# Kernel optimization log

Hardware: AMD Instinct MI355X
Metric: run time of the kernel (lower is better)

Reference implementation:

```python
import jax, jax.numpy as jnp
import numpy as np

B, T, N_EMBD, HEAD = 8, 2048, 1024, 64

def setup_inputs() -> dict:
    key = jax.random.key(0)
    kx, kk, kq, kv = jax.random.split(key, 4)
    x = jax.random.normal(kx, (B, T, N_EMBD), dtype=jnp.float32)
    Wk = jax.random.normal(kk, (HEAD, N_EMBD), dtype=jnp.float32) * 0.02
    Wq = jax.random.normal(kq, (HEAD, N_EMBD), dtype=jnp.float32) * 0.02
    Wv = jax.random.normal(kv, (HEAD, N_EMBD), dtype=jnp.float32) * 0.02
    return {"x": x, "Wk": Wk, "Wq": Wq, "Wv": Wv}

def reference(x, Wk, Wq, Wv):
    # x: [B, T, C]; Linear(n_embd, head_size, bias=False) => x @ W.T
    Bq, Tq, C = x.shape
    q = jnp.einsum('btc,hc->bth', x, Wq)  # [B, T, H]
    k = jnp.einsum('btc,hc->bth', x, Wk)
    v = jnp.einsum('btc,hc->bth', x, Wv)
    # NOTE: source scales by C**0.5 with C = n_embd (not head_size); preserved.
    scale = 1.0 / jnp.sqrt(jnp.float32(C))
    wei = jnp.einsum('bth,bsh->bts', q, k) * scale  # [B, T, T]
    # causal mask: allow key position s <= query position t
    causal = jnp.tril(jnp.ones((Tq, Tq), dtype=bool))
    wei = jnp.where(causal[None, :, :], wei, -jnp.inf)
    wei = jax.nn.softmax(wei, axis=-1)
    # dropout is identity at inference
    out = jnp.einsum('bts,bsh->bth', wei, v)  # [B, T, H]
    return out
```

## Files before the change

kernel.cpp:

```cpp
#include <hip/hip_runtime.h>

#define TB 2048
#define NB 8
#define CEMB 1024
#define HD 64
#define BT (NB*TB)
#define QSCALE 0.04508422f

typedef __attribute__((ext_vector_type(8))) short bf16x8;
typedef __attribute__((ext_vector_type(4))) short bf16x4;
typedef __attribute__((ext_vector_type(4))) float f32x4;

#define MFMA32(a, b, c) __builtin_amdgcn_mfma_f32_16x16x32_bf16(a, b, c, 0, 0, 0)
#define MFMA16(a, b, c) __builtin_amdgcn_mfma_f32_16x16x16bf16_1k(a, b, c, 0, 0, 0)

__device__ inline short f2bf(float f) {
    union { float f; unsigned u; } v; v.f = f;
    unsigned r = v.u + 0x7fffu + ((v.u >> 16) & 1u);
    return (short)(r >> 16);
}
__device__ inline float bf2f(short s) {
    union { unsigned u; float f; } v; v.u = ((unsigned)(unsigned short)s) << 16;
    return v.f;
}

__global__ __launch_bounds__(256) void wpack(const float* __restrict__ Wk,
                                             const float* __restrict__ Wq,
                                             const float* __restrict__ Wv,
                                             short* __restrict__ W2) {
    int c = blockIdx.x * 256 + threadIdx.x;
    int lane = c & 63, ntk = c >> 6;
    int nt = ntk % 12, kc = ntk / 12;
    int n = nt * 16 + (lane & 15);
    int col = kc * 32 + (lane >> 4) * 8;
    const float* src = (n < 64) ? Wk + n * 1024
                     : (n < 128) ? Wq + (n - 64) * 1024
                                 : Wv + (n - 128) * 1024;
    float4 a = *(const float4*)(src + col);
    float4 b = *(const float4*)(src + col + 4);
    bf16x8 o;
    o[0] = f2bf(a.x); o[1] = f2bf(a.y); o[2] = f2bf(a.z); o[3] = f2bf(a.w);
    o[4] = f2bf(b.x); o[5] = f2bf(b.y); o[6] = f2bf(b.z); o[7] = f2bf(b.w);
    *(bf16x8*)(W2 + (size_t)c * 8) = o;
}

__global__ __launch_bounds__(256) void qkv_proj(const float* __restrict__ x,
                                                const short* __restrict__ W2,
                                                short* __restrict__ Qb,
                                                short* __restrict__ Kb,
                                                short* __restrict__ Vt) {
    __shared__ short4 Lred[4][3][3][64];
    int tid = threadIdx.x, wave = tid >> 6, lane = tid & 63;
    int l15 = lane & 15, quad = lane >> 4;
    int m0 = blockIdx.x * 16;
    int mrow = m0 + l15;

    f32x4 acc[12];
#pragma unroll
    for (int i = 0; i < 12; ++i) acc[i] = f32x4{0.f, 0.f, 0.f, 0.f};

    const float4* xb4 = (const float4*)(x + (size_t)mrow * CEMB + wave * 256) + quad * 2;
    float4 xq[6];
    xq[0] = xb4[0];  xq[1] = xb4[1];
    xq[2] = xb4[8];  xq[3] = xb4[9];
    xq[4] = xb4[16]; xq[5] = xb4[17];

    const short* wbase = W2 + ((size_t)(wave * 8) * 12 * 64 + lane) * 8;
    bf16x8 wA[12], wB[12];
#pragma unroll
    for (int nt = 0; nt < 12; ++nt)
        wA[nt] = *(const bf16x8*)(wbase + nt * 512);

#pragma unroll
    for (int kc = 0; kc < 8; ++kc) {
        float4 x0 = xq[(kc % 3) * 2], x1 = xq[(kc % 3) * 2 + 1];
        if (kc + 1 < 8) {
            const short* wn = wbase + (size_t)(kc + 1) * 6144;
            if (kc & 1) {
#pragma unroll
                for (int nt = 0; nt < 12; ++nt) wA[nt] = *(const bf16x8*)(wn + nt * 512);
            } else {
#pragma unroll
                for (int nt = 0; nt < 12; ++nt) wB[nt] = *(const bf16x8*)(wn + nt * 512);
            }
        }
        if (kc + 3 < 8) {
            xq[((kc + 3) % 3) * 2]     = xb4[(kc + 3) * 8];
            xq[((kc + 3) % 3) * 2 + 1] = xb4[(kc + 3) * 8 + 1];
        }
        bf16x8 af;
        af[0] = f2bf(x0.x); af[1] = f2bf(x0.y); af[2] = f2bf(x0.z); af[3] = f2bf(x0.w);
        af[4] = f2bf(x1.x); af[5] = f2bf(x1.y); af[6] = f2bf(x1.z); af[7] = f2bf(x1.w);
        if (kc & 1) {
#pragma unroll
            for (int nt = 0; nt < 12; ++nt) acc[nt] = MFMA32(af, wB[nt], acc[nt]);
        } else {
#pragma unroll
            for (int nt = 0; nt < 12; ++nt) acc[nt] = MFMA32(af, wA[nt], acc[nt]);
        }
    }

#pragma unroll
    for (int nt = 0; nt < 12; ++nt) {
        int o = nt / 3;
        if (o != wave) {
            int rank = wave - (wave > o ? 1 : 0);
            short4 p;
            p.x = f2bf(acc[nt][0]); p.y = f2bf(acc[nt][1]);
            p.z = f2bf(acc[nt][2]); p.w = f2bf(acc[nt][3]);
            Lred[o][rank][nt % 3][lane] = p;
        }
    }
    __syncthreads();

    int b = blockIdx.x >> 7;
    int sblk = (m0 & 2047) >> 4;
#pragma unroll
    for (int nt = 0; nt < 12; ++nt) {
        if (wave == nt / 3) {
            f32x4 s = acc[nt];
#pragma unroll
            for (int rk = 0; rk < 3; ++rk) {
                short4 p = Lred[nt / 3][rk][nt % 3][lane];
                s[0] += bf2f(p.x); s[1] += bf2f(p.y);
                s[2] += bf2f(p.z); s[3] += bf2f(p.w);
            }
            if (nt < 4) {
                int h = nt * 16 + l15;
#pragma unroll
                for (int r = 0; r < 4; ++r)
                    Kb[(size_t)(m0 + quad * 4 + r) * HD + h] = f2bf(s[r]);
            } else if (nt < 8) {
                int h = (nt - 4) * 16 + l15;
#pragma unroll
                for (int r = 0; r < 4; ++r)
                    Qb[(size_t)(m0 + quad * 4 + r) * HD + h] = f2bf(s[r] * QSCALE);
            } else {
                int h = (nt - 8) * 16 + l15;
                short4 o4;
                o4.x = f2bf(s[0]); o4.y = f2bf(s[1]); o4.z = f2bf(s[2]); o4.w = f2bf(s[3]);
                *(short4*)(Vt + ((size_t)(b * 128 + sblk) * 64 + h) * 16 + quad * 4) = o4;
            }
        }
    }
}

__global__ __launch_bounds__(256) void flash(const short* __restrict__ Qb,
                                             const short* __restrict__ Kb,
                                             const short* __restrict__ Vt,
                                             float* __restrict__ out) {
    __shared__ float Of[4][16][68];
    __shared__ float Ml[4][16];
    int tid = threadIdx.x, wave = tid >> 6, lane = tid & 63;
    int l15 = lane & 15, quad = lane >> 4;
    int i = blockIdx.x;
    int round = i >> 8, s = i & 255;
    int b = round * 2 + (s & 1);
    int q = (round & 1) ? 127 - (s >> 1) : (s >> 1);
    int tq0 = q * 16;
    size_t bT = (size_t)b * TB;

    const short* qrow = Qb + (bT + tq0 + l15) * HD;
    bf16x8 qf0 = *(const bf16x8*)(qrow + quad * 8);
    bf16x8 qf1 = *(const bf16x8*)(qrow + 32 + quad * 8);

    bf16x4 ones4;
#pragma unroll
    for (int j = 0; j < 4; ++j) ones4[j] = (short)0x3F80;

    f32x4 accO[4];
#pragma unroll
    for (int k = 0; k < 4; ++k) accO[k] = f32x4{0.f, 0.f, 0.f, 0.f};
    f32x4 accL = f32x4{0.f, 0.f, 0.f, 0.f};

    int ntiles = (q + 4) >> 2;
    const short* kbase = Kb + bT * HD;
    const short* vtb = Vt + (size_t)b * 131072;

    int myt = wave;
    if (myt < ntiles) {
        bf16x8 kf[8];
        {
            const short* kr = kbase + (size_t)(myt * 64 + l15) * HD + quad * 8;
#pragma unroll
            for (int st = 0; st < 4; ++st) {
                kf[st * 2]     = *(const bf16x8*)(kr + (size_t)st * 16 * HD);
                kf[st * 2 + 1] = *(const bf16x8*)(kr + (size_t)st * 16 * HD + 32);
            }
        }
        for (; myt < ntiles; myt += 4) {
            int s0 = myt * 64;
            bf16x4 vf[16];
#pragma unroll
            for (int g = 0; g < 4; ++g) {
                int sb = (s0 >> 4) + g;
#pragma unroll
                for (int ht = 0; ht < 4; ++ht)
                    vf[g * 4 + ht] = *(const bf16x4*)(vtb + ((size_t)(sb * 64 + ht * 16 + l15)) * 16 + quad * 4);
            }
            f32x4 sv[4];
#pragma unroll
            for (int st = 0; st < 4; ++st) {
                f32x4 sacc = f32x4{0.f, 0.f, 0.f, 0.f};
                sacc = MFMA32(kf[st * 2], qf0, sacc);
                sacc = MFMA32(kf[st * 2 + 1], qf1, sacc);
                sv[st] = sacc;
            }
            if (myt + 4 < ntiles) {
                const short* kr = kbase + (size_t)(s0 + 256 + l15) * HD + quad * 8;
#pragma unroll
                for (int st = 0; st < 4; ++st) {
                    kf[st * 2]     = *(const bf16x8*)(kr + (size_t)st * 16 * HD);
                    kf[st * 2 + 1] = *(const bf16x8*)(kr + (size_t)st * 16 * HD + 32);
                }
            }
            bool full = (s0 + 64 <= tq0);
            int tg = tq0 + l15;
            bf16x4 pk[4];
#pragma unroll
            for (int st = 0; st < 4; ++st) {
#pragma unroll
                for (int r = 0; r < 4; ++r) {
                    int sg = s0 + st * 16 + quad * 4 + r;
                    float e = (full || sg <= tg) ? __builtin_amdgcn_exp2f(sv[st][r]) : 0.f;
                    pk[st][r] = f2bf(e);
                }
            }
#pragma unroll
            for (int g = 0; g < 4; ++g) {
                accL = MFMA16(ones4, pk[g], accL);
#pragma unroll
                for (int ht = 0; ht < 4; ++ht)
                    accO[ht] = MFMA16(vf[g * 4 + ht], pk[g], accO[ht]);
            }
        }
    }

#pragma unroll
    for (int ht = 0; ht < 4; ++ht) {
        float4 o4;
        o4.x = accO[ht][0]; o4.y = accO[ht][1]; o4.z = accO[ht][2]; o4.w = accO[ht][3];
        *(float4*)&Of[wave][l15][ht * 16 + quad * 4] = o4;
    }
    if (quad == 0) Ml[wave][l15] = accL[0];
    __syncthreads();

    int row = tid >> 4, c4 = (tid & 15) * 4;
    float L = Ml[0][row] + Ml[1][row] + Ml[2][row] + Ml[3][row];
    float inv = 1.0f / L;
    float4 p0 = *(const float4*)&Of[0][row][c4];
    float4 p1 = *(const float4*)&Of[1][row][c4];
    float4 p2 = *(const float4*)&Of[2][row][c4];
    float4 p3 = *(const float4*)&Of[3][row][c4];
    float4 o;
    o.x = (p0.x + p1.x + p2.x + p3.x) * inv;
    o.y = (p0.y + p1.y + p2.y + p3.y) * inv;
    o.z = (p0.z + p1.z + p2.z + p3.z) * inv;
    o.w = (p0.w + p1.w + p2.w + p3.w) * inv;
    *(float4*)(out + (bT + tq0 + row) * HD + c4) = o;
}

extern "C" void kernel_launch(void* const* d_in, const int* in_sizes, int n_in,
                              void* d_out, int out_size, void* d_ws, size_t ws_size,
                              hipStream_t stream) {
    const float* x  = (const float*)d_in[0];
    const float* Wk = (const float*)d_in[1];
    const float* Wq = (const float*)d_in[2];
    const float* Wv = (const float*)d_in[3];
    float* out = (float*)d_out;

    short* W2 = (short*)d_ws;
    short* Qb = W2 + 192 * 1024;
    short* Kb = Qb + (size_t)BT * HD;
    short* Vt = Kb + (size_t)BT * HD;

    wpack<<<96, 256, 0, stream>>>(Wk, Wq, Wv, W2);
    qkv_proj<<<1024, 256, 0, stream>>>(x, W2, Qb, Kb, Vt);
    flash<<<1024, 256, 0, stream>>>(Qb, Kb, Vt, out);
}
```

Before: 156.6 us.

## Process 32 rows per block in projection and attention to reuse weights and K/V

Both the QKV projection and the flash kernel now handle two 16-row tiles per block, so each loaded weight fragment or K/V tile feeds twice as many MFMAs. Grids are halved to 512 blocks. The V-transpose layout moves to 32-key blocks, which allows 16-byte loads. Causal masking is now decided per 16-key subtile, and the projection drops its double-buffered weight prefetch. The trade-offs are higher register pressure, fewer blocks for load balance and occupancy, and more exposed weight-load latency.

```diff
diff --git a/kernel.cpp b/kernel.cpp
--- a/kernel.cpp
+++ b/kernel.cpp
@@ -49,97 +49,96 @@
                                                 short* __restrict__ Qb,
                                                 short* __restrict__ Kb,
                                                 short* __restrict__ Vt) {
-    __shared__ short4 Lred[4][3][3][64];
+    __shared__ short4 Lred[4][3][6][64];
     int tid = threadIdx.x, wave = tid >> 6, lane = tid & 63;
     int l15 = lane & 15, quad = lane >> 4;
-    int m0 = blockIdx.x * 16;
-    int mrow = m0 + l15;
-
-    f32x4 acc[12];
-#pragma unroll
-    for (int i = 0; i < 12; ++i) acc[i] = f32x4{0.f, 0.f, 0.f, 0.f};
-
-    const float4* xb4 = (const float4*)(x + (size_t)mrow * CEMB + wave * 256) + quad * 2;
-    float4 xq[6];
-    xq[0] = xb4[0];  xq[1] = xb4[1];
-    xq[2] = xb4[8];  xq[3] = xb4[9];
-    xq[4] = xb4[16]; xq[5] = xb4[17];
+    int m0 = blockIdx.x * 32;
+
+    f32x4 acc[24];
+#pragma unroll
+    for (int i = 0; i < 24; ++i) acc[i] = f32x4{0.f, 0.f, 0.f, 0.f};
+
+    const float4* xA = (const float4*)(x + (size_t)(m0 + l15) * CEMB + wave * 256) + quad * 2;
+    const float4* xB = (const float4*)(x + (size_t)(m0 + 16 + l15) * CEMB + wave * 256) + quad * 2;
+    float4 xq[8];
+    xq[0] = xA[0]; xq[1] = xA[1]; xq[2] = xB[0]; xq[3] = xB[1];
+    xq[4] = xA[8]; xq[5] = xA[9]; xq[6] = xB[8]; xq[7] = xB[9];
 
     const short* wbase = W2 + ((size_t)(wave * 8) * 12 * 64 + lane) * 8;
-    bf16x8 wA[12], wB[12];
-#pragma unroll
-    for (int nt = 0; nt < 12; ++nt)
-        wA[nt] = *(const bf16x8*)(wbase + nt * 512);
-
 #pragma unroll
     for (int kc = 0; kc < 8; ++kc) {
-        float4 x0 = xq[(kc % 3) * 2], x1 = xq[(kc % 3) * 2 + 1];
-        if (kc + 1 < 8) {
-            const short* wn = wbase + (size_t)(kc + 1) * 6144;
-            if (kc & 1) {
-#pragma unroll
-                for (int nt = 0; nt < 12; ++nt) wA[nt] = *(const bf16x8*)(wn + nt * 512);
-            } else {
-#pragma unroll
-                for (int nt = 0; nt < 12; ++nt) wB[nt] = *(const bf16x8*)(wn + nt * 512);
-            }
-        }
-        if (kc + 3 < 8) {
-            xq[((kc + 3) % 3) * 2]     = xb4[(kc + 3) * 8];
-            xq[((kc + 3) % 3) * 2 + 1] = xb4[(kc + 3) * 8 + 1];
-        }
-        bf16x8 af;
-        af[0] = f2bf(x0.x); af[1] = f2bf(x0.y); af[2] = f2bf(x0.z); af[3] = f2bf(x0.w);
-        af[4] = f2bf(x1.x); af[5] = f2bf(x1.y); af[6] = f2bf(x1.z); af[7] = f2bf(x1.w);
-        if (kc & 1) {
-#pragma unroll
-            for (int nt = 0; nt < 12; ++nt) acc[nt] = MFMA32(af, wB[nt], acc[nt]);
-        } else {
-#pragma unroll
-            for (int nt = 0; nt < 12; ++nt) acc[nt] = MFMA32(af, wA[nt], acc[nt]);
+        bf16x8 wf[12];
+#pragma unroll
+        for (int nt = 0; nt < 12; ++nt)
+            wf[nt] = *(const bf16x8*)(wbase + (size_t)kc * 6144 + nt * 512);
+        int base = (kc & 1) * 4;
+        float4 a0 = xq[base], a1 = xq[base + 1];
+        float4 b0 = xq[base + 2], b1 = xq[base + 3];
+        if (kc + 2 < 8) {
+            xq[base]     = xA[(kc + 2) * 8]; xq[base + 1] = xA[(kc + 2) * 8 + 1];
+            xq[base + 2] = xB[(kc + 2) * 8]; xq[base + 3] = xB[(kc + 2) * 8 + 1];
+        }
+        bf16x8 af0, af1;
+        af0[0] = f2bf(a0.x); af0[1] = f2bf(a0.y); af0[2] = f2bf(a0.z); af0[3] = f2bf(a0.w);
+        af0[4] = f2bf(a1.x); af0[5] = f2bf(a1.y); af0[6] = f2bf(a1.z); af0[7] = f2bf(a1.w);
+        af1[0] = f2bf(b0.x); af1[1] = f2bf(b0.y); af1[2] = f2bf(b0.z); af1[3] = f2bf(b0.w);
+        af1[4] = f2bf(b1.x); af1[5] = f2bf(b1.y); af1[6] = f2bf(b1.z); af1[7] = f2bf(b1.w);
+#pragma unroll
+        for (int nt = 0; nt < 12; ++nt) {
+            acc[nt * 2]     = MFMA32(af0, wf[nt], acc[nt * 2]);
+            acc[nt * 2 + 1] = MFMA32(af1, wf[nt], acc[nt * 2 + 1]);
         }
     }
 
 #pragma unroll
     for (int nt = 0; nt < 12; ++nt) {
-        int o = nt / 3;
-        if (o != wave) {
-            int rank = wave - (wave > o ? 1 : 0);
-            short4 p;
-            p.x = f2bf(acc[nt][0]); p.y = f2bf(acc[nt][1]);
-            p.z = f2bf(acc[nt][2]); p.w = f2bf(acc[nt][3]);
-            Lred[o][rank][nt % 3][lane] = p;
+#pragma unroll
+        for (int mt = 0; mt < 2; ++mt) {
+            int o = nt / 3;
+            if (o != wave) {
+                int rank = wave - (wave > o ? 1 : 0);
+                short4 p;
+                p.x = f2bf(acc[nt * 2 + mt][0]); p.y = f2bf(acc[nt * 2 + mt][1]);
+                p.z = f2bf(acc[nt * 2 + mt][2]); p.w = f2bf(acc[nt * 2 + mt][3]);
+                Lred[o][rank][(nt % 3) * 2 + mt][lane] = p;
+            }
         }
     }
     __syncthreads();
 
-    int b = blockIdx.x >> 7;
-    int sblk = (m0 & 2047) >> 4;
+    int b = blockIdx.x >> 6;
+    int sblk32 = blockIdx.x & 63;
 #pragma unroll
     for (int nt = 0; nt < 12; ++nt) {
         if (wave == nt / 3) {
-            f32x4 s = acc[nt];
+            f32x4 s0 = acc[nt * 2], s1 = acc[nt * 2 + 1];
 #pragma unroll
             for (int rk = 0; rk < 3; ++rk) {
-                short4 p = Lred[nt / 3][rk][nt % 3][lane];
-                s[0] += bf2f(p.x); s[1] += bf2f(p.y);
-                s[2] += bf2f(p.z); s[3] += bf2f(p.w);
+                short4 p0 = Lred[nt / 3][rk][(nt % 3) * 2][lane];
+                short4 p1 = Lred[nt / 3][rk][(nt % 3) * 2 + 1][lane];
+                s0[0] += bf2f(p0.x); s0[1] += bf2f(p0.y); s0[2] += bf2f(p0.z); s0[3] += bf2f(p0.w);
+                s1[0] += bf2f(p1.x); s1[1] += bf2f(p1.y); s1[2] += bf2f(p1.z); s1[3] += bf2f(p1.w);
             }
             if (nt < 4) {
                 int h = nt * 16 + l15;
 #pragma unroll
-                for (int r = 0; r < 4; ++r)
-                    Kb[(size_t)(m0 + quad * 4 + r) * HD + h] = f2bf(s[r]);
+                for (int r = 0; r < 4; ++r) {
+                    Kb[(size_t)(m0 + quad * 4 + r) * HD + h]      = f2bf(s0[r]);
+                    Kb[(size_t)(m0 + 16 + quad * 4 + r) * HD + h] = f2bf(s1[r]);
+                }
             } else if (nt < 8) {
                 int h = (nt - 4) * 16 + l15;
 #pragma unroll
-                for (int r = 0; r < 4; ++r)
-                    Qb[(size_t)(m0 + quad * 4 + r) * HD + h] = f2bf(s[r] * QSCALE);
+                for (int r = 0; r < 4; ++r) {
+                    Qb[(size_t)(m0 + quad * 4 + r) * HD + h]      = f2bf(s0[r] * QSCALE);
+                    Qb[(size_t)(m0 + 16 + quad * 4 + r) * HD + h] = f2bf(s1[r] * QSCALE);
+                }
             } else {
                 int h = (nt - 8) * 16 + l15;
-                short4 o4;
-                o4.x = f2bf(s[0]); o4.y = f2bf(s[1]); o4.z = f2bf(s[2]); o4.w = f2bf(s[3]);
-                *(short4*)(Vt + ((size_t)(b * 128 + sblk) * 64 + h) * 16 + quad * 4) = o4;
+                bf16x8 v8;
+                v8[0] = f2bf(s0[0]); v8[1] = f2bf(s0[1]); v8[2] = f2bf(s0[2]); v8[3] = f2bf(s0[3]);
+                v8[4] = f2bf(s1[0]); v8[5] = f2bf(s1[1]); v8[6] = f2bf(s1[2]); v8[7] = f2bf(s1[3]);
+                *(bf16x8*)(Vt + ((size_t)((b * 64 + sblk32) * 64 + h)) * 32 + quad * 8) = v8;
             }
         }
     }
@@ -149,31 +148,35 @@
                                              const short* __restrict__ Kb,
                                              const short* __restrict__ Vt,
                                              float* __restrict__ out) {
-    __shared__ float Of[4][16][68];
-    __shared__ float Ml[4][16];
+    __shared__ float Of[4][2][16][68];
+    __shared__ float Ml[4][2][16];
     int tid = threadIdx.x, wave = tid >> 6, lane = tid & 63;
     int l15 = lane & 15, quad = lane >> 4;
     int i = blockIdx.x;
     int round = i >> 8, s = i & 255;
-    int b = round * 2 + (s & 1);
-    int q = (round & 1) ? 127 - (s >> 1) : (s >> 1);
-    int tq0 = q * 16;
+    int b = s & 7;
+    int g32 = s >> 3;
+    int q32 = round ? 63 - g32 : g32;
+    int tq0 = q32 * 32;
     size_t bT = (size_t)b * TB;
 
-    const short* qrow = Qb + (bT + tq0 + l15) * HD;
-    bf16x8 qf0 = *(const bf16x8*)(qrow + quad * 8);
-    bf16x8 qf1 = *(const bf16x8*)(qrow + 32 + quad * 8);
+    const short* qr0 = Qb + (bT + tq0 + l15) * HD;
+    const short* qr1 = Qb + (bT + tq0 + 16 + l15) * HD;
+    bf16x8 qf00 = *(const bf16x8*)(qr0 + quad * 8);
+    bf16x8 qf01 = *(const bf16x8*)(qr0 + 32 + quad * 8);
+    bf16x8 qf10 = *(const bf16x8*)(qr1 + quad * 8);
+    bf16x8 qf11 = *(const bf16x8*)(qr1 + 32 + quad * 8);
 
     bf16x4 ones4;
 #pragma unroll
     for (int j = 0; j < 4; ++j) ones4[j] = (short)0x3F80;
 
-    f32x4 accO[4];
-#pragma unroll
-    for (int k = 0; k < 4; ++k) accO[k] = f32x4{0.f, 0.f, 0.f, 0.f};
-    f32x4 accL = f32x4{0.f, 0.f, 0.f, 0.f};
-
-    int ntiles = (q + 4) >> 2;
+    f32x4 accO0[4], accO1[4];
+#pragma unroll
+    for (int k = 0; k < 4; ++k) { accO0[k] = f32x4{0.f,0.f,0.f,0.f}; accO1[k] = f32x4{0.f,0.f,0.f,0.f}; }
+    f32x4 accL0 = f32x4{0.f,0.f,0.f,0.f}, accL1 = f32x4{0.f,0.f,0.f,0.f};
+
+    int ntiles = (tq0 + 95) >> 6;
     const short* kbase = Kb + bT * HD;
     const short* vtb = Vt + (size_t)b * 131072;
 
@@ -190,21 +193,22 @@
         }
         for (; myt < ntiles; myt += 4) {
             int s0 = myt * 64;
-            bf16x4 vf[16];
-#pragma unroll
-            for (int g = 0; g < 4; ++g) {
-                int sb = (s0 >> 4) + g;
+            bf16x8 vf8[8];
+#pragma unroll
+            for (int sb2 = 0; sb2 < 2; ++sb2)
 #pragma unroll
                 for (int ht = 0; ht < 4; ++ht)
-                    vf[g * 4 + ht] = *(const bf16x4*)(vtb + ((size_t)(sb * 64 + ht * 16 + l15)) * 16 + quad * 4);
-            }
-            f32x4 sv[4];
+                    vf8[sb2 * 4 + ht] = *(const bf16x8*)(
+                        vtb + ((size_t)(((s0 >> 5) + sb2) * 64 + ht * 16 + l15)) * 32 + quad * 8);
+            f32x4 sv0[4], sv1[4];
 #pragma unroll
             for (int st = 0; st < 4; ++st) {
-                f32x4 sacc = f32x4{0.f, 0.f, 0.f, 0.f};
-                sacc = MFMA32(kf[st * 2], qf0, sacc);
-                sacc = MFMA32(kf[st * 2 + 1], qf1, sacc);
-                sv[st] = sacc;
+                f32x4 t0 = f32x4{0.f,0.f,0.f,0.f}, t1 = f32x4{0.f,0.f,0.f,0.f};
+                t0 = MFMA32(kf[st * 2], qf00, t0);
+                t0 = MFMA32(kf[st * 2 + 1], qf01, t0);
+                t1 = MFMA32(kf[st * 2], qf10, t1);
+                t1 = MFMA32(kf[st * 2 + 1], qf11, t1);
+                sv0[st] = t0; sv1[st] = t1;
             }
             if (myt + 4 < ntiles) {
                 const short* kr = kbase + (size_t)(s0 + 256 + l15) * HD + quad * 8;
@@ -214,50 +218,65 @@
                     kf[st * 2 + 1] = *(const bf16x8*)(kr + (size_t)st * 16 * HD + 32);
                 }
             }
-            bool full = (s0 + 64 <= tq0);
-            int tg = tq0 + l15;
-            bf16x4 pk[4];
+            int t0g = tq0 + l15, t1g = tq0 + 16 + l15;
+            bf16x4 pk0[4], pk1[4];
 #pragma unroll
             for (int st = 0; st < 4; ++st) {
+                bool full0 = (s0 + st * 16 + 15 <= tq0);
+                bool full1 = (s0 + st * 16 + 15 <= tq0 + 16);
 #pragma unroll
                 for (int r = 0; r < 4; ++r) {
                     int sg = s0 + st * 16 + quad * 4 + r;
-                    float e = (full || sg <= tg) ? __builtin_amdgcn_exp2f(sv[st][r]) : 0.f;
-                    pk[st][r] = f2bf(e);
+                    float e0 = (full0 || sg <= t0g) ? __builtin_amdgcn_exp2f(sv0[st][r]) : 0.f;
+                    float e1 = (full1 || sg <= t1g) ? __builtin_amdgcn_exp2f(sv1[st][r]) : 0.f;
+                    pk0[st][r] = f2bf(e0);
+                    pk1[st][r] = f2bf(e1);
                 }
             }
 #pragma unroll
             for (int g = 0; g < 4; ++g) {
-                accL = MFMA16(ones4, pk[g], accL);
-#pragma unroll
-                for (int ht = 0; ht < 4; ++ht)
-                    accO[ht] = MFMA16(vf[g * 4 + ht], pk[g], accO[ht]);
+                accL0 = MFMA16(ones4, pk0[g], accL0);
+                accL1 = MFMA16(ones4, pk1[g], accL1);
+#pragma unroll
+                for (int ht = 0; ht < 4; ++ht) {
+                    bf16x8 v = vf8[(g >> 1) * 4 + ht];
+                    bf16x4 va;
+                    if (g & 1) { va[0] = v[4]; va[1] = v[5]; va[2] = v[6]; va[3] = v[7]; }
+                    else       { va[0] = v[0]; va[1] = v[1]; va[2] = v[2]; va[3] = v[3]; }
+                    accO0[ht] = MFMA16(va, pk0[g], accO0[ht]);
+                    accO1[ht] = MFMA16(va, pk1[g], accO1[ht]);
+                }
             }
         }
     }
 
 #pragma unroll
     for (int ht = 0; ht < 4; ++ht) {
-        float4 o4;
-        o4.x = accO[ht][0]; o4.y = accO[ht][1]; o4.z = accO[ht][2]; o4.w = accO[ht][3];
-        *(float4*)&Of[wave][l15][ht * 16 + quad * 4] = o4;
-    }
-    if (quad == 0) Ml[wave][l15] = accL[0];
+        float4 o0, o1;
+        o0.x = accO0[ht][0]; o0.y = accO0[ht][1]; o0.z = accO0[ht][2]; o0.w = accO0[ht][3];
+        o1.x = accO1[ht][0]; o1.y = accO1[ht][1]; o1.z = accO1[ht][2]; o1.w = accO1[ht][3];
+        *(float4*)&Of[wave][0][l15][ht * 16 + quad * 4] = o0;
+        *(float4*)&Of[wave][1][l15][ht * 16 + quad * 4] = o1;
+    }
+    if (quad == 0) { Ml[wave][0][l15] = accL0[0]; Ml[wave][1][l15] = accL1[0]; }
     __syncthreads();
 
     int row = tid >> 4, c4 = (tid & 15) * 4;
-    float L = Ml[0][row] + Ml[1][row] + Ml[2][row] + Ml[3][row];
-    float inv = 1.0f / L;
-    float4 p0 = *(const float4*)&Of[0][row][c4];
-    float4 p1 = *(const float4*)&Of[1][row][c4];
-    float4 p2 = *(const float4*)&Of[2][row][c4];
-    float4 p3 = *(const float4*)&Of[3][row][c4];
-    float4 o;
-    o.x = (p0.x + p1.x + p2.x + p3.x) * inv;
-    o.y = (p0.y + p1.y + p2.y + p3.y) * inv;
-    o.z = (p0.z + p1.z + p2.z + p3.z) * inv;
-    o.w = (p0.w + p1.w + p2.w + p3.w) * inv;
-    *(float4*)(out + (bT + tq0 + row) * HD + c4) = o;
+#pragma unroll
+    for (int qt = 0; qt < 2; ++qt) {
+        float L = Ml[0][qt][row] + Ml[1][qt][row] + Ml[2][qt][row] + Ml[3][qt][row];
+        float inv = 1.0f / L;
+        float4 p0 = *(const float4*)&Of[0][qt][row][c4];
+        float4 p1 = *(const float4*)&Of[1][qt][row][c4];
+        float4 p2 = *(const float4*)&Of[2][qt][row][c4];
+        float4 p3 = *(const float4*)&Of[3][qt][row][c4];
+        float4 o;
+        o.x = (p0.x + p1.x + p2.x + p3.x) * inv;
+        o.y = (p0.y + p1.y + p2.y + p3.y) * inv;
+        o.z = (p0.z + p1.z + p2.z + p3.z) * inv;
+        o.w = (p0.w + p1.w + p2.w + p3.w) * inv;
+        *(float4*)(out + (bT + tq0 + qt * 16 + row) * HD + c4) = o;
+    }
 }
 
 extern "C" void kernel_launch(void* const* d_in, const int* in_sizes, int n_in,
@@ -275,6 +294,6 @@
     short* Vt = Kb + (size_t)BT * HD;
 
     wpack<<<96, 256, 0, stream>>>(Wk, Wq, Wv, W2);
-    qkv_proj<<<1024, 256, 0, stream>>>(x, W2, Qb, Kb, Vt);
-    flash<<<1024, 256, 0, stream>>>(Qb, Kb, Vt, out);
-}
+    qkv_proj<<<512, 256, 0, stream>>>(x, W2, Qb, Kb, Vt);
+    flash<<<512, 256, 0, stream>>>(Qb, Kb, Vt, out);
+}
```

After: 140.6 us. 10.3% less time.
